# Performance work log

Measured on AMD Instinct MI355X. Metric: run time of the kernel, lower is better.

## Reference

```python
import jax, jax.numpy as jnp
import numpy as np

D = 1024; H = 16; HD = 64; L = 8; V = 2048; FF = 4096; WIN = 256
THETA = 10000.0; EPS = 1e-5; LN_EPS = 1e-5; MAXCYC = 16
NM = 16; NR = 72; NT = 12; ME = 64; RE = 64; TE = 32; TPE = 16; DE = 16
B = 2; S = 1024


def _rotate_half(x):
    # torch: stack((-x[...,1::2], x[...,0::2]), -1).flatten(-2)
    x1 = x[..., ::2]
    x2 = x[..., 1::2]
    return jnp.stack((-x2, x1), axis=-1).reshape(x.shape)


def _rmsnorm(x, w):
    return w * (x * jax.lax.rsqrt(jnp.mean(x * x, axis=-1, keepdims=True) + EPS))


def _layernorm(x, g, b):
    mu = jnp.mean(x, axis=-1, keepdims=True)
    var = jnp.mean((x - mu) ** 2, axis=-1, keepdims=True)
    return (x - mu) * jax.lax.rsqrt(var + LN_EPS) * g + b


def setup_inputs() -> dict:
    key = jax.random.key(0)
    ks = iter(jax.random.split(key, 64))
    w = lambda shape: jax.random.normal(next(ks), shape, jnp.float32) * 0.02
    inp = {
        'tokens': jax.random.randint(next(ks), (B, S), 0, V),
        'mood': jax.random.randint(next(ks), (B,), 0, NM),
        'raga': jax.random.randint(next(ks), (B,), 0, NR),
        'taal': jax.random.randint(next(ks), (B,), 0, NT),
        'tempo': jax.random.uniform(next(ks), (B,), jnp.float32),
        'duration': jax.random.uniform(next(ks), (B,), jnp.float32),
        'taal_cycle_len': 8,
        'tok_emb': w((V, D)),
        'mood_emb': w((NM, ME)), 'raga_emb': w((NR, RE)), 'taal_emb': w((NT, TE)),
        'tempo_w': w((TPE, 1)), 'tempo_b': jnp.zeros((TPE,), jnp.float32),
        'dur_w': w((DE, 1)), 'dur_b': jnp.zeros((DE,), jnp.float32),
        'proj_w': w((D, ME + RE + TE + TPE + DE)), 'proj_b': jnp.zeros((D,), jnp.float32),
        'ln_g': jnp.ones((D,), jnp.float32), 'ln_b': jnp.zeros((D,), jnp.float32),
        'cycle_emb': w((MAXCYC, D)), 'strength_emb': w((4, D)),
        'l_anorm': jnp.ones((L, D), jnp.float32), 'l_fnorm': jnp.ones((L, D), jnp.float32),
        'l_q': w((L, D, D)), 'l_k': w((L, D, D)), 'l_v': w((L, D, D)), 'l_o': w((L, D, D)),
        'l_w1': w((L, FF, D)), 'l_w2': w((L, D, FF)), 'l_w3': w((L, FF, D)),
        'final_norm': jnp.ones((D,), jnp.float32),
        'head_w': w((V, D)),
    }
    return inp


def reference(tokens, mood, raga, taal, tempo, duration, taal_cycle_len,
              tok_emb, mood_emb, raga_emb, taal_emb, tempo_w, tempo_b, dur_w, dur_b,
              proj_w, proj_b, ln_g, ln_b, cycle_emb, strength_emb,
              l_anorm, l_fnorm, l_q, l_k, l_v, l_o, l_w1, l_w2, l_w3,
              final_norm, head_w):
    bsz, seq_len = tokens.shape
    # --- ConditioningModule ---
    tp = tempo[:, None] * tempo_w[:, 0][None, :] + tempo_b      # Linear(1, TPE)
    dp = duration[:, None] * dur_w[:, 0][None, :] + dur_b       # Linear(1, DE)
    cond = jnp.concatenate([mood_emb[mood], raga_emb[raga], taal_emb[taal], tp, dp], axis=-1)
    cond = jax.nn.gelu(cond @ proj_w.T + proj_b, approximate=False)
    cond = _layernorm(cond, ln_g, ln_b)                          # [B, D]
    # --- TaalPositionEncoder (taal_cycle_len is static python int) ---
    cyc = min(int(taal_cycle_len), MAXCYC)
    pos_emb = cycle_emb[jnp.arange(seq_len) % cyc]
    strengths = jnp.full((seq_len,), 3, jnp.int32).at[::int(taal_cycle_len)].set(0)
    taal_pos = pos_emb + strength_emb[strengths]                 # [S, D]
    # --- input embedding ---
    x = tok_emb[tokens] + cond[:, None, :] + taal_pos[None]      # [B, S, D]
    # --- RoPE tables (scaling=1.0) ---
    inv_freq = 1.0 / (THETA ** (jnp.arange(0, HD, 2, jnp.float32) / HD))
    freqs = jnp.outer(jnp.arange(seq_len, dtype=jnp.float32), inv_freq)
    emb = jnp.concatenate([freqs, freqs], axis=-1)               # [S, HD]
    cos = jnp.cos(emb)[None, None]
    sin = jnp.sin(emb)[None, None]
    # --- causal sliding-window mask bias ---
    idx = jnp.arange(seq_len)
    allow = (idx[:, None] >= idx[None, :]) & (idx[:, None] - idx[None, :] < WIN)
    bias = jnp.where(allow, 0.0, -jnp.inf).astype(x.dtype)       # [S, S]
    scale = 1.0 / np.sqrt(HD)

    def block(x, p):
        an, fn, qw, kw, vw, ow, w1, w2, w3 = p
        h = _rmsnorm(x, an)
        q = (h @ qw.T).reshape(bsz, seq_len, H, HD).transpose(0, 2, 1, 3)
        k = (h @ kw.T).reshape(bsz, seq_len, H, HD).transpose(0, 2, 1, 3)
        v = (h @ vw.T).reshape(bsz, seq_len, H, HD).transpose(0, 2, 1, 3)
        q = q * cos + _rotate_half(q) * sin
        k = k * cos + _rotate_half(k) * sin
        scores = jnp.einsum('bhqd,bhkd->bhqk', q, k) * scale + bias
        attn = jax.nn.softmax(scores, axis=-1)
        y = jnp.einsum('bhqk,bhkd->bhqd', attn, v)
        y = y.transpose(0, 2, 1, 3).reshape(bsz, seq_len, D)
        x = x + y @ ow.T
        h2 = _rmsnorm(x, fn)
        x = x + (jax.nn.silu(h2 @ w1.T) * (h2 @ w3.T)) @ w2.T
        return x, None

    x, _ = jax.lax.scan(block, x, (l_anorm, l_fnorm, l_q, l_k, l_v, l_o, l_w1, l_w2, l_w3))
    x = _rmsnorm(x, final_norm)
    return x @ head_w.T                                          # [B, S, V] logits
```

## Files before the change

kernel.cpp:

```cpp
#include <hip/hip_runtime.h>
#include <math.h>

#define D_ 1024
#define H_ 16
#define HD_ 64
#define L_ 8
#define V_ 2048
#define FF_ 4096
#define WIN_ 256
#define B_ 2
#define S_ 1024
#define MAXCYC_ 16

typedef __attribute__((ext_vector_type(4))) float f32x4;
typedef __attribute__((ext_vector_type(8))) short s16x8;

__device__ __forceinline__ unsigned short f2bf(float f) {
  union { float f; unsigned int u; } v; v.f = f;
  unsigned int r = v.u + 0x7FFFu + ((v.u >> 16) & 1u);
  return (unsigned short)(r >> 16);
}

__device__ __forceinline__ float wave_sum(float v) {
  #pragma unroll
  for (int m = 1; m < 64; m <<= 1) v += __shfl_xor(v, m, 64);
  return v;
}

__device__ __forceinline__ void gload16(const unsigned short* g, unsigned short* lds) {
  __builtin_amdgcn_global_load_lds(
      (const __attribute__((address_space(1))) void*)g,
      (__attribute__((address_space(3))) void*)lds,
      16, 0, 0);
}

__global__ __launch_bounds__(256) void cvt_kernel(
    const float* __restrict__ src, unsigned short* __restrict__ dst, int n8)
{
  int i = blockIdx.x*256 + threadIdx.x;
  if (i >= n8) return;
  const float4* s = (const float4*)src + (size_t)i*2;
  float4 a = s[0], b = s[1];
  ushort4 lo, hi;
  lo.x = f2bf(a.x); lo.y = f2bf(a.y); lo.z = f2bf(a.z); lo.w = f2bf(a.w);
  hi.x = f2bf(b.x); hi.y = f2bf(b.y); hi.z = f2bf(b.z); hi.w = f2bf(b.w);
  *(ushort4*)(dst + (size_t)i*8)     = lo;
  *(ushort4*)(dst + (size_t)i*8 + 4) = hi;
}

__global__ __launch_bounds__(256) void cond_kernel(
    const int* mood, const int* raga, const int* taal,
    const float* tempo, const float* duration,
    const float* mood_emb, const float* raga_emb, const float* taal_emb,
    const float* tempo_w, const float* tempo_b, const float* dur_w, const float* dur_b,
    const float* proj_w, const float* proj_b, const float* ln_g, const float* ln_b,
    float* cond)
{
  int b = blockIdx.x;
  int t = threadIdx.x;
  __shared__ float feat[192];
  __shared__ float red[4];
  if (t < 64)        feat[t] = mood_emb[mood[b]*64 + t];
  else if (t < 128)  feat[t] = raga_emb[raga[b]*64 + (t-64)];
  else if (t < 160)  feat[t] = taal_emb[taal[b]*32 + (t-128)];
  else if (t < 176)  feat[t] = tempo[b]*tempo_w[t-160] + tempo_b[t-160];
  else if (t < 192)  feat[t] = duration[b]*dur_w[t-176] + dur_b[t-176];
  __syncthreads();
  float g[4];
  #pragma unroll
  for (int r = 0; r < 4; ++r) {
    int j = t + 256*r;
    const float* w = proj_w + (size_t)j*192;
    float acc = proj_b[j];
    for (int f = 0; f < 192; ++f) acc += feat[f]*w[f];
    g[r] = 0.5f * acc * (1.0f + erff(acc * 0.7071067811865475f));
  }
  int lane = t & 63, wv = t >> 6;
  float s1 = g[0]+g[1]+g[2]+g[3];
  s1 = wave_sum(s1);
  if (lane == 0) red[wv] = s1;
  __syncthreads();
  float mu = (red[0]+red[1]+red[2]+red[3]) * (1.0f/1024.0f);
  __syncthreads();
  float vs = 0.f;
  #pragma unroll
  for (int r = 0; r < 4; ++r) { float d = g[r]-mu; vs += d*d; }
  vs = wave_sum(vs);
  if (lane == 0) red[wv] = vs;
  __syncthreads();
  float var = (red[0]+red[1]+red[2]+red[3]) * (1.0f/1024.0f);
  float is = rsqrtf(var + 1e-5f);
  #pragma unroll
  for (int r = 0; r < 4; ++r) {
    int j = t + 256*r;
    cond[(size_t)b*D_ + j] = (g[r]-mu)*is*ln_g[j] + ln_b[j];
  }
}

__global__ __launch_bounds__(256) void embed_kernel(
    const int* tokens, const float* tok_emb, const float* cond,
    const float* cycle_emb, const float* strength_emb, const int* tcl_p, float* x)
{
  int row = blockIdx.x;
  int b = row >> 10, s = row & 1023;
  int tcl = tcl_p[0];
  int cyc = tcl < MAXCYC_ ? tcl : MAXCYC_;
  int pr  = s % cyc;
  int str = (s % tcl == 0) ? 0 : 3;
  int tok = tokens[row];
  int d = threadIdx.x * 4;
  float4 a = *(const float4*)&tok_emb[(size_t)tok*D_ + d];
  float4 c = *(const float4*)&cond[(size_t)b*D_ + d];
  float4 p = *(const float4*)&cycle_emb[(size_t)pr*D_ + d];
  float4 e = *(const float4*)&strength_emb[(size_t)str*D_ + d];
  float4 o; o.x=a.x+c.x+p.x+e.x; o.y=a.y+c.y+p.y+e.y; o.z=a.z+c.z+p.z+e.z; o.w=a.w+c.w+p.w+e.w;
  *(float4*)&x[(size_t)row*D_ + d] = o;
}

__global__ __launch_bounds__(256) void rmsnorm_kernel(
    const float* x, const float* w, unsigned short* out)
{
  int row = blockIdx.x;
  int t = threadIdx.x;
  __shared__ float red[4];
  const float* xr = x + (size_t)row*D_;
  float4 v = *(const float4*)&xr[t*4];
  float ss = v.x*v.x + v.y*v.y + v.z*v.z + v.w*v.w;
  ss = wave_sum(ss);
  int lane = t & 63, wv = t >> 6;
  if (lane == 0) red[wv] = ss;
  __syncthreads();
  float total = red[0]+red[1]+red[2]+red[3];
  float scale = rsqrtf(total * (1.0f/1024.0f) + 1e-5f);
  float4 wv4 = *(const float4*)&w[t*4];
  ushort4 o;
  o.x = f2bf(wv4.x * v.x * scale);
  o.y = f2bf(wv4.y * v.y * scale);
  o.z = f2bf(wv4.z * v.z * scale);
  o.w = f2bf(wv4.w * v.w * scale);
  *(ushort4*)&out[(size_t)row*D_ + t*4] = o;
}

__global__ __launch_bounds__(256) void resid_rmsnorm_kernel(
    float* __restrict__ x, const float* __restrict__ part, int nparts,
    const float* __restrict__ w, unsigned short* __restrict__ out)
{
  int row = blockIdx.x;
  int t = threadIdx.x;
  __shared__ float red[4];
  size_t base = (size_t)row*D_ + t*4;
  const size_t pstride = (size_t)B_*S_*D_;
  float4 v = *(const float4*)&x[base];
  for (int p = 0; p < nparts; ++p) {
    float4 a = *(const float4*)&part[p*pstride + base];
    v.x += a.x; v.y += a.y; v.z += a.z; v.w += a.w;
  }
  *(float4*)&x[base] = v;
  float ss = v.x*v.x + v.y*v.y + v.z*v.z + v.w*v.w;
  ss = wave_sum(ss);
  int lane = t & 63, wv = t >> 6;
  if (lane == 0) red[wv] = ss;
  __syncthreads();
  float total = red[0]+red[1]+red[2]+red[3];
  float scale = rsqrtf(total * (1.0f/1024.0f) + 1e-5f);
  float4 wv4 = *(const float4*)&w[t*4];
  ushort4 o;
  o.x = f2bf(wv4.x * v.x * scale);
  o.y = f2bf(wv4.y * v.y * scale);
  o.z = f2bf(wv4.z * v.z * scale);
  o.w = f2bf(wv4.w * v.w * scale);
  *(ushort4*)&out[(size_t)row*D_ + t*4] = o;
}

__global__ __launch_bounds__(256) void rope_table_kernel(float* costab, float* sintab)
{
  int i = blockIdx.x*256 + threadIdx.x;
  int s = i >> 6, d = i & 63;
  float inv = powf(10000.0f, -(float)(d & 31) * (1.0f/32.0f));
  float ang = (float)s * inv;
  float sn, cs;
  sincosf(ang, &sn, &cs);
  costab[i] = cs; sintab[i] = sn;
}

__global__ __launch_bounds__(256) void attn_mfma(
    const unsigned short* __restrict__ q, const unsigned short* __restrict__ k,
    const unsigned short* __restrict__ v, unsigned short* __restrict__ y)
{
  __shared__ unsigned short Ks[64*64];
  __shared__ unsigned short VsT[64*72];
  __shared__ unsigned short Ps[4*16*72];

  int qb0 = blockIdx.x * 64;
  int h = blockIdx.y, b = blockIdx.z;
  int t = threadIdx.x, lane = t & 63, wv = t >> 6;
  int c = lane & 15, q4 = lane >> 4;
  unsigned short* Pw = &Ps[wv*16*72];

  s16x8 aq[2];
  {
    const unsigned short* qp =
        q + ((size_t)(b*S_ + qb0 + wv*16 + c)*D_ + h*HD_ + q4*8);
    aq[0] = *(const s16x8*)qp;
    aq[1] = *(const s16x8*)(qp + 32);
  }

  f32x4 o[4];
  #pragma unroll
  for (int j = 0; j < 4; ++j) o[j] = (f32x4){0.f,0.f,0.f,0.f};
  float m[4] = {-1e30f,-1e30f,-1e30f,-1e30f};
  float l[4] = {0.f,0.f,0.f,0.f};

  int skey = t >> 2;
  int scol = (t & 3) * 16;
  int kt0 = qb0 - 256; if (kt0 < 0) kt0 = 0;

  for (int kt = kt0; kt <= qb0; kt += 64) {
    __syncthreads();
    {
      const unsigned short* kp = k + ((size_t)(b*S_ + kt + skey)*D_ + h*HD_ + scol);
      s16x8 k0 = *(const s16x8*)kp;
      s16x8 k1 = *(const s16x8*)(kp + 8);
      int ch0 = scol >> 3;
      *(s16x8*)((char*)Ks + skey*128 + ((ch0 ^ (skey & 7)) << 4)) = k0;
      *(s16x8*)((char*)Ks + skey*128 + (((ch0+1) ^ (skey & 7)) << 4)) = k1;
      const unsigned short* vp = v + ((size_t)(b*S_ + kt + skey)*D_ + h*HD_ + scol);
      s16x8 v0 = *(const s16x8*)vp;
      s16x8 v1 = *(const s16x8*)(vp + 8);
      #pragma unroll
      for (int i = 0; i < 8; ++i) {
        VsT[(scol + i)*72 + skey]     = (unsigned short)v0[i];
        VsT[(scol + 8 + i)*72 + skey] = (unsigned short)v1[i];
      }
    }
    __syncthreads();

    f32x4 sa[4];
    #pragma unroll
    for (int j = 0; j < 4; ++j) sa[j] = (f32x4){0.f,0.f,0.f,0.f};
    __builtin_amdgcn_s_setprio(1);
    #pragma unroll
    for (int ks = 0; ks < 2; ++ks)
      #pragma unroll
      for (int j = 0; j < 4; ++j) {
        int key = j*16 + c;
        s16x8 bk = *(const s16x8*)((const char*)Ks + key*128 +
                                   (((q4 + ks*4) ^ (key & 7)) << 4));
        sa[j] = __builtin_amdgcn_mfma_f32_16x16x32_bf16(aq[ks], bk, sa[j], 0, 0, 0);
      }
    __builtin_amdgcn_s_setprio(0);

    float sv[4][4];
    #pragma unroll
    for (int j = 0; j < 4; ++j) {
      int kg = kt + j*16 + c;
      #pragma unroll
      for (int reg = 0; reg < 4; ++reg) {
        int qg = qb0 + wv*16 + q4*4 + reg;
        bool ok = (qg >= kg) && (qg - kg < WIN_);
        sv[j][reg] = ok ? sa[j][reg]*0.125f : -3e38f;
      }
    }
    #pragma unroll
    for (int reg = 0; reg < 4; ++reg) {
      float mx = fmaxf(fmaxf(sv[0][reg], sv[1][reg]), fmaxf(sv[2][reg], sv[3][reg]));
      #pragma unroll
      for (int msk = 1; msk < 16; msk <<= 1)
        mx = fmaxf(mx, __shfl_xor(mx, msk, 64));
      float nm = fmaxf(m[reg], mx);
      float f = __expf(m[reg] - nm);
      m[reg] = nm;
      l[reg] *= f;
      o[0][reg] *= f; o[1][reg] *= f; o[2][reg] *= f; o[3][reg] *= f;
      float ps = 0.f;
      #pragma unroll
      for (int j = 0; j < 4; ++j) {
        float p = __expf(sv[j][reg] - nm);
        ps += p;
        Pw[(q4*4 + reg)*72 + j*16 + c] = f2bf(p);
      }
      l[reg] += ps;
    }

    __builtin_amdgcn_s_setprio(1);
    #pragma unroll
    for (int ks = 0; ks < 2; ++ks) {
      s16x8 pa = *(const s16x8*)((const char*)Pw + c*144 + (q4 + ks*4)*16);
      #pragma unroll
      for (int j = 0; j < 4; ++j) {
        s16x8 bv = *(const s16x8*)((const char*)VsT + (j*16 + c)*144 + (q4 + ks*4)*16);
        o[j] = __builtin_amdgcn_mfma_f32_16x16x32_bf16(pa, bv, o[j], 0, 0, 0);
      }
    }
    __builtin_amdgcn_s_setprio(0);
  }

  float inv[4];
  #pragma unroll
  for (int reg = 0; reg < 4; ++reg) {
    float ll = l[reg];
    #pragma unroll
    for (int msk = 1; msk < 16; msk <<= 1) ll += __shfl_xor(ll, msk, 64);
    inv[reg] = 1.0f / ll;
  }
  #pragma unroll
  for (int j = 0; j < 4; ++j)
    #pragma unroll
    for (int reg = 0; reg < 4; ++reg)
      Pw[(q4*4 + reg)*72 + j*16 + c] = f2bf(o[j][reg] * inv[reg]);
  int lr = lane >> 2, cc = (lane & 3)*16;
  s16x8 y0 = *(const s16x8*)((const char*)Pw + lr*144 + cc*2);
  s16x8 y1 = *(const s16x8*)((const char*)Pw + lr*144 + cc*2 + 16);
  unsigned short* yp = y + ((size_t)(b*S_ + qb0 + wv*16 + lr)*D_ + h*HD_ + cc);
  *(s16x8*)yp = y0;
  *(s16x8*)(yp + 8) = y1;
}

__global__ __launch_bounds__(256, 2) void gemm_w13(
    const unsigned short* __restrict__ A,
    const unsigned short* __restrict__ W1, const unsigned short* __restrict__ W3,
    unsigned short* __restrict__ T, int K, int lda, int ldw)
{
  __shared__ unsigned short sA[3][128*32];
  __shared__ unsigned short sW1[3][128*32];
  __shared__ unsigned short sW3[3][128*32];
  int tid = threadIdx.x, lane = tid & 63, wave = tid >> 6;
  int wr = (wave >> 1)*64, wc = (wave & 1)*64;
  size_t bm = (size_t)blockIdx.x*128, bn = (size_t)blockIdx.y*128;
  int fr = lane & 15, q4 = lane >> 4, fq = q4*4;
  int lrow = lane >> 2;
  int gcol = ((lane & 3) ^ ((lrow >> 1) & 3)) * 8;

  f32x4 a1[4][4], a3[4][4];
  #pragma unroll
  for (int i = 0; i < 4; ++i)
    #pragma unroll
    for (int j = 0; j < 4; ++j) {
      a1[i][j] = (f32x4){0.f,0.f,0.f,0.f};
      a3[i][j] = (f32x4){0.f,0.f,0.f,0.f};
    }

  auto stage = [&](int buf, int kt) {
    #pragma unroll
    for (int p = 0; p < 2; ++p) {
      int seg = wave*2 + p;
      size_t row = (size_t)(seg*16 + lrow);
      gload16(A  + (bm + row)*(size_t)lda + kt + gcol, &sA[buf][seg*512]);
      gload16(W1 + (bn + row)*(size_t)ldw + kt + gcol, &sW1[buf][seg*512]);
      gload16(W3 + (bn + row)*(size_t)ldw + kt + gcol, &sW3[buf][seg*512]);
    }
  };

  int nt = K >> 5;
  stage(0, 0);
  stage(1, 32);
  for (int t = 0; t < nt; ++t) {
    int cur = t % 3;
    if (t + 2 < nt) {
      stage((t+2)%3, (t+2)*32);
      asm volatile("s_waitcnt vmcnt(12)" ::: "memory");
    } else if (t + 1 < nt) {
      asm volatile("s_waitcnt vmcnt(6)" ::: "memory");
    } else {
      asm volatile("s_waitcnt vmcnt(0)" ::: "memory");
    }
    __builtin_amdgcn_sched_barrier(0);
    __builtin_amdgcn_s_barrier();
    __builtin_amdgcn_sched_barrier(0);
    s16x8 af[4], b1[4], b3[4];
    #pragma unroll
    for (int i = 0; i < 4; ++i) {
      int ra = wr + i*16 + fr, rb = wc + i*16 + fr;
      af[i] = *(const s16x8*)((const char*)&sA[cur][0]  + ra*64 + ((q4 ^ ((ra>>1)&3)) << 4));
      b1[i] = *(const s16x8*)((const char*)&sW1[cur][0] + rb*64 + ((q4 ^ ((rb>>1)&3)) << 4));
      b3[i] = *(const s16x8*)((const char*)&sW3[cur][0] + rb*64 + ((q4 ^ ((rb>>1)&3)) << 4));
    }
    __builtin_amdgcn_s_setprio(1);
    #pragma unroll
    for (int i = 0; i < 4; ++i)
      #pragma unroll
      for (int j = 0; j < 4; ++j) {
        a1[i][j] = __builtin_amdgcn_mfma_f32_16x16x32_bf16(af[i], b1[j], a1[i][j], 0, 0, 0);
        a3[i][j] = __builtin_amdgcn_mfma_f32_16x16x32_bf16(af[i], b3[j], a3[i][j], 0, 0, 0);
      }
    __builtin_amdgcn_s_setprio(0);
    __builtin_amdgcn_sched_barrier(0);
    __builtin_amdgcn_s_barrier();
    __builtin_amdgcn_sched_barrier(0);
  }

  #pragma unroll
  for (int i = 0; i < 4; ++i)
    #pragma unroll
    for (int j = 0; j < 4; ++j) {
      size_t row0 = bm + wr + i*16 + fq;
      size_t col  = bn + wc + j*16 + fr;
      #pragma unroll
      for (int qi = 0; qi < 4; ++qi) {
        float u = a1[i][j][qi];
        float g = a3[i][j][qi];
        float su = u / (1.0f + __expf(-u));
        T[(row0 + qi)*(size_t)FF_ + col] = f2bf(su * g);
      }
    }
}

template<int EPI>
__device__ __forceinline__ void gemm64_core(
    const unsigned short* __restrict__ A, const unsigned short* __restrict__ W,
    float* __restrict__ Cf, unsigned short* __restrict__ Cb,
    int kbase, int Kslice, int lda, int ldw, int ldc,
    const float* __restrict__ costab, const float* __restrict__ sintab)
{
  __shared__ unsigned short sA[3][128*32];
  __shared__ unsigned short sW[3][64*32];
  int tid = threadIdx.x, lane = tid & 63, wave = tid >> 6;
  int wr = (wave >> 1)*64, wc = (wave & 1)*32;
  size_t bm = (size_t)blockIdx.x*128, bn = (size_t)blockIdx.y*64;
  int fr = lane & 15, q4 = lane >> 4, fq = q4*4;
  int lrow = lane >> 2;
  int gcol = ((lane & 3) ^ ((lrow >> 1) & 3)) * 8;

  f32x4 acc[4][2];
  #pragma unroll
  for (int i = 0; i < 4; ++i) {
    acc[i][0] = (f32x4){0.f,0.f,0.f,0.f};
    acc[i][1] = (f32x4){0.f,0.f,0.f,0.f};
  }

  auto stage = [&](int buf, int kt) {
    #pragma unroll
    for (int p = 0; p < 2; ++p) {
      int seg = wave*2 + p;
      gload16(A + (bm + seg*16 + lrow)*(size_t)lda + kt + gcol, &sA[buf][seg*512]);
    }
    gload16(W + (bn + wave*16 + lrow)*(size_t)ldw + kt + gcol, &sW[buf][wave*512]);
  };

  int nt = Kslice >> 5;
  stage(0, kbase);
  stage(1, kbase + 32);
  for (int t = 0; t < nt; ++t) {
    int cur = t % 3;
    if (t + 2 < nt) {
      stage((t+2)%3, kbase + (t+2)*32);
      asm volatile("s_waitcnt vmcnt(6)" ::: "memory");
    } else if (t + 1 < nt) {
      asm volatile("s_waitcnt vmcnt(3)" ::: "memory");
    } else {
      asm volatile("s_waitcnt vmcnt(0)" ::: "memory");
    }
    __builtin_amdgcn_sched_barrier(0);
    __builtin_amdgcn_s_barrier();
    __builtin_amdgcn_sched_barrier(0);
    s16x8 af[4], bw[2];
    #pragma unroll
    for (int i = 0; i < 4; ++i) {
      int r = wr + i*16 + fr;
      af[i] = *(const s16x8*)((const char*)&sA[cur][0] + r*64 + ((q4 ^ ((r>>1)&3)) << 4));
    }
    #pragma unroll
    for (int j = 0; j < 2; ++j) {
      int r = wc + j*16 + fr;
      bw[j] = *(const s16x8*)((const char*)&sW[cur][0] + r*64 + ((q4 ^ ((r>>1)&3)) << 4));
    }
    __builtin_amdgcn_s_setprio(1);
    #pragma unroll
    for (int i = 0; i < 4; ++i)
      #pragma unroll
      for (int j = 0; j < 2; ++j)
        acc[i][j] = __builtin_amdgcn_mfma_f32_16x16x32_bf16(af[i], bw[j], acc[i][j], 0, 0, 0);
    __builtin_amdgcn_s_setprio(0);
    __builtin_amdgcn_sched_barrier(0);
    __builtin_amdgcn_s_barrier();
    __builtin_amdgcn_sched_barrier(0);
  }

  #pragma unroll
  for (int i = 0; i < 4; ++i)
    #pragma unroll
    for (int j = 0; j < 2; ++j) {
      size_t row0 = bm + wr + i*16 + fq;
      size_t col  = bn + wc + j*16 + fr;
      #pragma unroll
      for (int qi = 0; qi < 4; ++qi) {
        float val = acc[i][j][qi];
        size_t idx = (row0 + qi)*(size_t)ldc + col;
        if (EPI == 3) {
          float pv = __shfl_xor(val, 1, 64);
          int srow = (int)((row0 + qi) & 1023);
          int d = (int)(col & 63);
          float cs = costab[srow*64 + d];
          float sn = sintab[srow*64 + d];
          Cb[idx] = f2bf(val*cs + ((d & 1) ? pv : -pv)*sn);
        } else if (EPI == 4) {
          Cb[idx] = f2bf(val);
        } else {
          Cf[idx] = val;
        }
      }
    }
}

template<int EPI>
__global__ __launch_bounds__(256, 3) void gemm64(
    const unsigned short* __restrict__ A, const unsigned short* __restrict__ W,
    float* __restrict__ Cf, int K, int lda, int ldw, int ldc)
{
  gemm64_core<EPI>(A, W, Cf, nullptr, 0, K, lda, ldw, ldc, nullptr, nullptr);
}

__global__ __launch_bounds__(256, 3) void gemm64_ksplit(
    const unsigned short* __restrict__ A, const unsigned short* __restrict__ W,
    float* __restrict__ P, int Kslice, int lda, int ldw, int ldc)
{
  float* out = P + (size_t)blockIdx.z * (size_t)B_ * S_ * ldc;
  gemm64_core<0>(A, W, out, nullptr, blockIdx.z*Kslice, Kslice, lda, ldw, ldc,
                 nullptr, nullptr);
}

__global__ __launch_bounds__(256, 3) void gemm_qkv64(
    const unsigned short* __restrict__ A,
    const unsigned short* __restrict__ Wq, const unsigned short* __restrict__ Wk,
    const unsigned short* __restrict__ Wv,
    unsigned short* __restrict__ Cq, unsigned short* __restrict__ Ck,
    unsigned short* __restrict__ Cv,
    const float* __restrict__ costab, const float* __restrict__ sintab)
{
  if (blockIdx.z == 0)
    gemm64_core<3>(A, Wq, nullptr, Cq, 0, D_, D_, D_, D_, costab, sintab);
  else if (blockIdx.z == 1)
    gemm64_core<3>(A, Wk, nullptr, Ck, 0, D_, D_, D_, D_, costab, sintab);
  else
    gemm64_core<4>(A, Wv, nullptr, Cv, 0, D_, D_, D_, D_, nullptr, nullptr);
}

extern "C" void kernel_launch(void* const* d_in, const int* in_sizes, int n_in,
                              void* d_out, int out_size, void* d_ws, size_t ws_size,
                              hipStream_t stream)
{
  const int*   tokens    = (const int*)d_in[0];
  const int*   mood      = (const int*)d_in[1];
  const int*   raga      = (const int*)d_in[2];
  const int*   taal      = (const int*)d_in[3];
  const float* tempo     = (const float*)d_in[4];
  const float* duration  = (const float*)d_in[5];
  const int*   tcl       = (const int*)d_in[6];
  const float* tok_emb   = (const float*)d_in[7];
  const float* mood_emb  = (const float*)d_in[8];
  const float* raga_emb  = (const float*)d_in[9];
  const float* taal_emb  = (const float*)d_in[10];
  const float* tempo_w   = (const float*)d_in[11];
  const float* tempo_b   = (const float*)d_in[12];
  const float* dur_w     = (const float*)d_in[13];
  const float* dur_b     = (const float*)d_in[14];
  const float* proj_w    = (const float*)d_in[15];
  const float* proj_b    = (const float*)d_in[16];
  const float* ln_g      = (const float*)d_in[17];
  const float* ln_b      = (const float*)d_in[18];
  const float* cycle_emb = (const float*)d_in[19];
  const float* strength_e= (const float*)d_in[20];
  const float* l_anorm   = (const float*)d_in[21];
  const float* l_fnorm   = (const float*)d_in[22];
  const float* l_q       = (const float*)d_in[23];
  const float* l_k       = (const float*)d_in[24];
  const float* l_v       = (const float*)d_in[25];
  const float* l_o       = (const float*)d_in[26];
  const float* l_w1      = (const float*)d_in[27];
  const float* l_w2      = (const float*)d_in[28];
  const float* l_w3      = (const float*)d_in[29];
  const float* final_norm= (const float*)d_in[30];
  const float* head_w    = (const float*)d_in[31];

  size_t off = 0;
  char* wsb = (char*)d_ws;
  auto alloc = [&](size_t bytes) -> char* {
    char* p = wsb + off;
    off += (bytes + 255) & ~(size_t)255;
    return p;
  };
  float*          condb  = (float*)alloc((size_t)B_*D_*4);
  float*          costab = (float*)alloc((size_t)S_*HD_*4);
  float*          sintab = (float*)alloc((size_t)S_*HD_*4);
  float*          x      = (float*)alloc((size_t)B_*S_*D_*4);
  unsigned short* hbuf   = (unsigned short*)alloc((size_t)B_*S_*D_*2);
  unsigned short* qb     = (unsigned short*)alloc((size_t)B_*S_*D_*2);
  unsigned short* kb     = (unsigned short*)alloc((size_t)B_*S_*D_*2);
  unsigned short* vb     = (unsigned short*)alloc((size_t)B_*S_*D_*2);
  unsigned short* yb     = (unsigned short*)alloc((size_t)B_*S_*D_*2);
  unsigned short* tb     = (unsigned short*)alloc((size_t)B_*S_*FF_*2);
  float*          pbuf   = (float*)alloc((size_t)4*B_*S_*D_*4);

  const size_t N_QKVO = (size_t)L_*D_*D_;
  const size_t N_FF   = (size_t)L_*FF_*D_;
  const size_t N_HEAD = (size_t)V_*D_;
  unsigned short* wbf = (unsigned short*)alloc((4*N_QKVO + 3*N_FF + N_HEAD)*2);
  unsigned short* bq = wbf;
  unsigned short* bk = wbf + N_QKVO;
  unsigned short* bv = wbf + 2*N_QKVO;
  unsigned short* bo = wbf + 3*N_QKVO;
  unsigned short* b1 = wbf + 4*N_QKVO;
  unsigned short* b2 = wbf + 4*N_QKVO + N_FF;
  unsigned short* b3 = wbf + 4*N_QKVO + 2*N_FF;
  unsigned short* bh = wbf + 4*N_QKVO + 3*N_FF;

  rope_table_kernel<<<(S_*HD_)/256, 256, 0, stream>>>(costab, sintab);
  cond_kernel<<<B_, 256, 0, stream>>>(mood, raga, taal, tempo, duration,
      mood_emb, raga_emb, taal_emb, tempo_w, tempo_b, dur_w, dur_b,
      proj_w, proj_b, ln_g, ln_b, condb);
  embed_kernel<<<B_*S_, 256, 0, stream>>>(tokens, tok_emb, condb, cycle_emb,
      strength_e, tcl, x);

  cvt_kernel<<<(int)(N_QKVO/8/256), 256, 0, stream>>>(l_q,  bq, (int)(N_QKVO/8));
  cvt_kernel<<<(int)(N_QKVO/8/256), 256, 0, stream>>>(l_k,  bk, (int)(N_QKVO/8));
  cvt_kernel<<<(int)(N_QKVO/8/256), 256, 0, stream>>>(l_v,  bv, (int)(N_QKVO/8));
  cvt_kernel<<<(int)(N_QKVO/8/256), 256, 0, stream>>>(l_o,  bo, (int)(N_QKVO/8));
  cvt_kernel<<<(int)(N_FF/8/256),   256, 0, stream>>>(l_w1, b1, (int)(N_FF/8));
  cvt_kernel<<<(int)(N_FF/8/256),   256, 0, stream>>>(l_w2, b2, (int)(N_FF/8));
  cvt_kernel<<<(int)(N_FF/8/256),   256, 0, stream>>>(l_w3, b3, (int)(N_FF/8));
  cvt_kernel<<<(int)(N_HEAD/8/256), 256, 0, stream>>>(head_w, bh, (int)(N_HEAD/8));

  const int rows = B_*S_;
  rmsnorm_kernel<<<rows, 256, 0, stream>>>(x, l_anorm, hbuf);
  for (int l = 0; l < L_; ++l) {
    size_t dd = (size_t)l*D_*D_;
    size_t fd = (size_t)l*FF_*D_;
    gemm_qkv64<<<dim3(rows/128, D_/64, 3), 256, 0, stream>>>(
        hbuf, bq + dd, bk + dd, bv + dd, qb, kb, vb, costab, sintab);
    attn_mfma<<<dim3(S_/64, H_, B_), 256, 0, stream>>>(qb, kb, vb, yb);
    gemm64_ksplit<<<dim3(rows/128, D_/64, 2), 256, 0, stream>>>(
        yb, bo + dd, pbuf, 512, D_, D_, D_);
    resid_rmsnorm_kernel<<<rows, 256, 0, stream>>>(
        x, pbuf, 2, l_fnorm + (size_t)l*D_, hbuf);
    gemm_w13<<<dim3(rows/128, FF_/128), 256, 0, stream>>>(
        hbuf, b1 + fd, b3 + fd, tb, D_, D_, D_);
    gemm64_ksplit<<<dim3(rows/128, D_/64, 4), 256, 0, stream>>>(
        tb, b2 + fd, pbuf, 1024, FF_, FF_, D_);
    const float* nextw = (l+1 < L_) ? (l_anorm + (size_t)(l+1)*D_) : final_norm;
    resid_rmsnorm_kernel<<<rows, 256, 0, stream>>>(x, pbuf, 4, nextw, hbuf);
  }
  gemm64<0><<<dim3(rows/128, V_/64), 256, 0, stream>>>(
      hbuf, bh, (float*)d_out, D_, D_, D_, V_);
}
```

Measured before the change: 1.583 ms.

## Widen GEMM tiles to 128x128 and process 128 queries per attention block

The shared GEMM core moves from 128x64 to 128x128 output tiles, giving each wave a 4x4 grid of MFMA accumulators and more operand reuse per LDS load. The wait counts and grid sizes are updated to match. The output-projection k-split grows from 2 to 4 slices so the grid stays large enough, and the residual kernel now sums 4 partials. Attention blocks now cover 128 queries with two 16-row groups per wave, so K/V tiles are shared by twice as many queries, and waves skip tiles outside their window. The costs are higher register pressure, fewer blocks per launch (the attention grid is halved), and extra partial-sum traffic for the output projection.

New measurement: 1.717 ms. 8.4% more time.

```diff
diff --git a/kernel.cpp b/kernel.cpp
--- a/kernel.cpp
+++ b/kernel.cpp
@@ -189,33 +189,41 @@
 {
   __shared__ unsigned short Ks[64*64];
   __shared__ unsigned short VsT[64*72];
-  __shared__ unsigned short Ps[4*16*72];
-
-  int qb0 = blockIdx.x * 64;
+  __shared__ unsigned short Ps[4*32*72];
+
+  int qb0 = blockIdx.x * 128;
   int h = blockIdx.y, b = blockIdx.z;
   int t = threadIdx.x, lane = t & 63, wv = t >> 6;
   int c = lane & 15, q4 = lane >> 4;
-  unsigned short* Pw = &Ps[wv*16*72];
-
-  s16x8 aq[2];
-  {
+  unsigned short* Pw = &Ps[wv*32*72];
+  int qbase = qb0 + wv*32;
+
+  s16x8 aq[2][2];
+  #pragma unroll
+  for (int rg = 0; rg < 2; ++rg) {
     const unsigned short* qp =
-        q + ((size_t)(b*S_ + qb0 + wv*16 + c)*D_ + h*HD_ + q4*8);
-    aq[0] = *(const s16x8*)qp;
-    aq[1] = *(const s16x8*)(qp + 32);
-  }
-
-  f32x4 o[4];
-  #pragma unroll
-  for (int j = 0; j < 4; ++j) o[j] = (f32x4){0.f,0.f,0.f,0.f};
-  float m[4] = {-1e30f,-1e30f,-1e30f,-1e30f};
-  float l[4] = {0.f,0.f,0.f,0.f};
+        q + ((size_t)(b*S_ + qbase + rg*16 + c)*D_ + h*HD_ + q4*8);
+    aq[rg][0] = *(const s16x8*)qp;
+    aq[rg][1] = *(const s16x8*)(qp + 32);
+  }
+
+  f32x4 o[2][4];
+  float m[2][4], l[2][4];
+  #pragma unroll
+  for (int rg = 0; rg < 2; ++rg)
+    #pragma unroll
+    for (int j = 0; j < 4; ++j) {
+      o[rg][j] = (f32x4){0.f,0.f,0.f,0.f};
+      m[rg][j] = -1e30f; l[rg][j] = 0.f;
+    }
 
   int skey = t >> 2;
   int scol = (t & 3) * 16;
-  int kt0 = qb0 - 256; if (kt0 < 0) kt0 = 0;
-
-  for (int kt = kt0; kt <= qb0; kt += 64) {
+  int kt0 = qb0 - (WIN_-1); if (kt0 < 0) kt0 = 0;
+  kt0 &= ~63;
+  int ktend = qb0 + 64;
+
+  for (int kt = kt0; kt <= ktend; kt += 64) {
     __syncthreads();
     {
       const unsigned short* kp = k + ((size_t)(b*S_ + kt + skey)*D_ + h*HD_ + scol);
@@ -235,85 +243,94 @@
     }
     __syncthreads();
 
-    f32x4 sa[4];
-    #pragma unroll
-    for (int j = 0; j < 4; ++j) sa[j] = (f32x4){0.f,0.f,0.f,0.f};
-    __builtin_amdgcn_s_setprio(1);
-    #pragma unroll
-    for (int ks = 0; ks < 2; ++ks)
+    if (kt > qbase + 31 || kt + 63 < qbase - (WIN_-1)) continue;
+
+    #pragma unroll
+    for (int rg = 0; rg < 2; ++rg) {
+      f32x4 sa[4];
+      #pragma unroll
+      for (int j = 0; j < 4; ++j) sa[j] = (f32x4){0.f,0.f,0.f,0.f};
+      __builtin_amdgcn_s_setprio(1);
+      #pragma unroll
+      for (int ks = 0; ks < 2; ++ks)
+        #pragma unroll
+        for (int j = 0; j < 4; ++j) {
+          int key = j*16 + c;
+          s16x8 bk = *(const s16x8*)((const char*)Ks + key*128 +
+                                     (((q4 + ks*4) ^ (key & 7)) << 4));
+          sa[j] = __builtin_amdgcn_mfma_f32_16x16x32_bf16(aq[rg][ks], bk, sa[j], 0, 0, 0);
+        }
+      __builtin_amdgcn_s_setprio(0);
+
+      float sv[4][4];
       #pragma unroll
       for (int j = 0; j < 4; ++j) {
-        int key = j*16 + c;
-        s16x8 bk = *(const s16x8*)((const char*)Ks + key*128 +
-                                   (((q4 + ks*4) ^ (key & 7)) << 4));
-        sa[j] = __builtin_amdgcn_mfma_f32_16x16x32_bf16(aq[ks], bk, sa[j], 0, 0, 0);
+        int kg = kt + j*16 + c;
+        #pragma unroll
+        for (int reg = 0; reg < 4; ++reg) {
+          int qg = qbase + rg*16 + q4*4 + reg;
+          bool ok = (qg >= kg) && (qg - kg < WIN_);
+          sv[j][reg] = ok ? sa[j][reg]*0.125f : -3e38f;
+        }
       }
-    __builtin_amdgcn_s_setprio(0);
-
-    float sv[4][4];
-    #pragma unroll
-    for (int j = 0; j < 4; ++j) {
-      int kg = kt + j*16 + c;
       #pragma unroll
       for (int reg = 0; reg < 4; ++reg) {
-        int qg = qb0 + wv*16 + q4*4 + reg;
-        bool ok = (qg >= kg) && (qg - kg < WIN_);
-        sv[j][reg] = ok ? sa[j][reg]*0.125f : -3e38f;
+        float mx = fmaxf(fmaxf(sv[0][reg], sv[1][reg]), fmaxf(sv[2][reg], sv[3][reg]));
+        #pragma unroll
+        for (int msk = 1; msk < 16; msk <<= 1)
+          mx = fmaxf(mx, __shfl_xor(mx, msk, 64));
+        float nm = fmaxf(m[rg][reg], mx);
+        float f = __expf(m[rg][reg] - nm);
+        m[rg][reg] = nm;
+        l[rg][reg] *= f;
+        o[rg][0][reg] *= f; o[rg][1][reg] *= f;
+        o[rg][2][reg] *= f; o[rg][3][reg] *= f;
+        float ps = 0.f;
+        #pragma unroll
+        for (int j = 0; j < 4; ++j) {
+          float p = __expf(sv[j][reg] - nm);
+          ps += p;
+          Pw[(rg*16 + q4*4 + reg)*72 + j*16 + c] = f2bf(p);
+        }
+        l[rg][reg] += ps;
       }
-    }
+
+      __builtin_amdgcn_s_setprio(1);
+      #pragma unroll
+      for (int ks = 0; ks < 2; ++ks) {
+        s16x8 pa = *(const s16x8*)((const char*)Pw + (rg*16 + c)*144 + (q4 + ks*4)*16);
+        #pragma unroll
+        for (int j = 0; j < 4; ++j) {
+          s16x8 bv = *(const s16x8*)((const char*)VsT + (j*16 + c)*144 + (q4 + ks*4)*16);
+          o[rg][j] = __builtin_amdgcn_mfma_f32_16x16x32_bf16(pa, bv, o[rg][j], 0, 0, 0);
+        }
+      }
+      __builtin_amdgcn_s_setprio(0);
+    }
+  }
+
+  #pragma unroll
+  for (int rg = 0; rg < 2; ++rg) {
     #pragma unroll
     for (int reg = 0; reg < 4; ++reg) {
-      float mx = fmaxf(fmaxf(sv[0][reg], sv[1][reg]), fmaxf(sv[2][reg], sv[3][reg]));
-      #pragma unroll
-      for (int msk = 1; msk < 16; msk <<= 1)
-        mx = fmaxf(mx, __shfl_xor(mx, msk, 64));
-      float nm = fmaxf(m[reg], mx);
-      float f = __expf(m[reg] - nm);
-      m[reg] = nm;
-      l[reg] *= f;
-      o[0][reg] *= f; o[1][reg] *= f; o[2][reg] *= f; o[3][reg] *= f;
-      float ps = 0.f;
-      #pragma unroll
-      for (int j = 0; j < 4; ++j) {
-        float p = __expf(sv[j][reg] - nm);
-        ps += p;
-        Pw[(q4*4 + reg)*72 + j*16 + c] = f2bf(p);
-      }
-      l[reg] += ps;
-    }
-
-    __builtin_amdgcn_s_setprio(1);
-    #pragma unroll
-    for (int ks = 0; ks < 2; ++ks) {
-      s16x8 pa = *(const s16x8*)((const char*)Pw + c*144 + (q4 + ks*4)*16);
-      #pragma unroll
-      for (int j = 0; j < 4; ++j) {
-        s16x8 bv = *(const s16x8*)((const char*)VsT + (j*16 + c)*144 + (q4 + ks*4)*16);
-        o[j] = __builtin_amdgcn_mfma_f32_16x16x32_bf16(pa, bv, o[j], 0, 0, 0);
-      }
-    }
-    __builtin_amdgcn_s_setprio(0);
-  }
-
-  float inv[4];
-  #pragma unroll
-  for (int reg = 0; reg < 4; ++reg) {
-    float ll = l[reg];
-    #pragma unroll
-    for (int msk = 1; msk < 16; msk <<= 1) ll += __shfl_xor(ll, msk, 64);
-    inv[reg] = 1.0f / ll;
-  }
-  #pragma unroll
-  for (int j = 0; j < 4; ++j)
-    #pragma unroll
-    for (int reg = 0; reg < 4; ++reg)
-      Pw[(q4*4 + reg)*72 + j*16 + c] = f2bf(o[j][reg] * inv[reg]);
+      float ll = l[rg][reg];
+      #pragma unroll
+      for (int msk = 1; msk < 16; msk <<= 1) ll += __shfl_xor(ll, msk, 64);
+      float inv = 1.0f / ll;
+      #pragma unroll
+      for (int j = 0; j < 4; ++j)
+        Pw[(rg*16 + q4*4 + reg)*72 + j*16 + c] = f2bf(o[rg][j][reg] * inv);
+    }
+  }
   int lr = lane >> 2, cc = (lane & 3)*16;
-  s16x8 y0 = *(const s16x8*)((const char*)Pw + lr*144 + cc*2);
-  s16x8 y1 = *(const s16x8*)((const char*)Pw + lr*144 + cc*2 + 16);
-  unsigned short* yp = y + ((size_t)(b*S_ + qb0 + wv*16 + lr)*D_ + h*HD_ + cc);
-  *(s16x8*)yp = y0;
-  *(s16x8*)(yp + 8) = y1;
+  #pragma unroll
+  for (int rg = 0; rg < 2; ++rg) {
+    s16x8 y0 = *(const s16x8*)((const char*)Pw + (rg*16 + lr)*144 + cc*2);
+    s16x8 y1 = *(const s16x8*)((const char*)Pw + (rg*16 + lr)*144 + cc*2 + 16);
+    unsigned short* yp = y + ((size_t)(b*S_ + qbase + rg*16 + lr)*D_ + h*HD_ + cc);
+    *(s16x8*)yp = y0;
+    *(s16x8*)(yp + 8) = y1;
+  }
 }
 
 __global__ __launch_bounds__(256, 2) void gemm_w13(
@@ -406,35 +423,36 @@
 }
 
 template<int EPI>
-__device__ __forceinline__ void gemm64_core(
+__device__ __forceinline__ void gemm128_core(
     const unsigned short* __restrict__ A, const unsigned short* __restrict__ W,
     float* __restrict__ Cf, unsigned short* __restrict__ Cb,
     int kbase, int Kslice, int lda, int ldw, int ldc,
     const float* __restrict__ costab, const float* __restrict__ sintab)
 {
   __shared__ unsigned short sA[3][128*32];
-  __shared__ unsigned short sW[3][64*32];
+  __shared__ unsigned short sW[3][128*32];
   int tid = threadIdx.x, lane = tid & 63, wave = tid >> 6;
-  int wr = (wave >> 1)*64, wc = (wave & 1)*32;
-  size_t bm = (size_t)blockIdx.x*128, bn = (size_t)blockIdx.y*64;
+  int wr = (wave >> 1)*64, wc = (wave & 1)*64;
+  size_t bm = (size_t)blockIdx.x*128, bn = (size_t)blockIdx.y*128;
   int fr = lane & 15, q4 = lane >> 4, fq = q4*4;
   int lrow = lane >> 2;
   int gcol = ((lane & 3) ^ ((lrow >> 1) & 3)) * 8;
 
-  f32x4 acc[4][2];
-  #pragma unroll
-  for (int i = 0; i < 4; ++i) {
-    acc[i][0] = (f32x4){0.f,0.f,0.f,0.f};
-    acc[i][1] = (f32x4){0.f,0.f,0.f,0.f};
-  }
+  f32x4 acc[4][4];
+  #pragma unroll
+  for (int i = 0; i < 4; ++i)
+    #pragma unroll
+    for (int j = 0; j < 4; ++j)
+      acc[i][j] = (f32x4){0.f,0.f,0.f,0.f};
 
   auto stage = [&](int buf, int kt) {
     #pragma unroll
     for (int p = 0; p < 2; ++p) {
       int seg = wave*2 + p;
-      gload16(A + (bm + seg*16 + lrow)*(size_t)lda + kt + gcol, &sA[buf][seg*512]);
-    }
-    gload16(W + (bn + wave*16 + lrow)*(size_t)ldw + kt + gcol, &sW[buf][wave*512]);
+      size_t row = (size_t)(seg*16 + lrow);
+      gload16(A + (bm + row)*(size_t)lda + kt + gcol, &sA[buf][seg*512]);
+      gload16(W + (bn + row)*(size_t)ldw + kt + gcol, &sW[buf][seg*512]);
+    }
   };
 
   int nt = Kslice >> 5;
@@ -444,31 +462,27 @@
     int cur = t % 3;
     if (t + 2 < nt) {
       stage((t+2)%3, kbase + (t+2)*32);
-      asm volatile("s_waitcnt vmcnt(6)" ::: "memory");
+      asm volatile("s_waitcnt vmcnt(8)" ::: "memory");
     } else if (t + 1 < nt) {
-      asm volatile("s_waitcnt vmcnt(3)" ::: "memory");
+      asm volatile("s_waitcnt vmcnt(4)" ::: "memory");
     } else {
       asm volatile("s_waitcnt vmcnt(0)" ::: "memory");
     }
     __builtin_amdgcn_sched_barrier(0);
     __builtin_amdgcn_s_barrier();
     __builtin_amdgcn_sched_barrier(0);
-    s16x8 af[4], bw[2];
+    s16x8 af[4], bw[4];
     #pragma unroll
     for (int i = 0; i < 4; ++i) {
-      int r = wr + i*16 + fr;
-      af[i] = *(const s16x8*)((const char*)&sA[cur][0] + r*64 + ((q4 ^ ((r>>1)&3)) << 4));
-    }
-    #pragma unroll
-    for (int j = 0; j < 2; ++j) {
-      int r = wc + j*16 + fr;
-      bw[j] = *(const s16x8*)((const char*)&sW[cur][0] + r*64 + ((q4 ^ ((r>>1)&3)) << 4));
+      int ra = wr + i*16 + fr, rb = wc + i*16 + fr;
+      af[i] = *(const s16x8*)((const char*)&sA[cur][0] + ra*64 + ((q4 ^ ((ra>>1)&3)) << 4));
+      bw[i] = *(const s16x8*)((const char*)&sW[cur][0] + rb*64 + ((q4 ^ ((rb>>1)&3)) << 4));
     }
     __builtin_amdgcn_s_setprio(1);
     #pragma unroll
     for (int i = 0; i < 4; ++i)
       #pragma unroll
-      for (int j = 0; j < 2; ++j)
+      for (int j = 0; j < 4; ++j)
         acc[i][j] = __builtin_amdgcn_mfma_f32_16x16x32_bf16(af[i], bw[j], acc[i][j], 0, 0, 0);
     __builtin_amdgcn_s_setprio(0);
     __builtin_amdgcn_sched_barrier(0);
@@ -479,7 +493,7 @@
   #pragma unroll
   for (int i = 0; i < 4; ++i)
     #pragma unroll
-    for (int j = 0; j < 2; ++j) {
+    for (int j = 0; j < 4; ++j) {
       size_t row0 = bm + wr + i*16 + fq;
       size_t col  = bn + wc + j*16 + fr;
       #pragma unroll
@@ -503,23 +517,23 @@
 }
 
 template<int EPI>
-__global__ __launch_bounds__(256, 3) void gemm64(
+__global__ __launch_bounds__(256, 3) void gemm128(
     const unsigned short* __restrict__ A, const unsigned short* __restrict__ W,
     float* __restrict__ Cf, int K, int lda, int ldw, int ldc)
 {
-  gemm64_core<EPI>(A, W, Cf, nullptr, 0, K, lda, ldw, ldc, nullptr, nullptr);
-}
-
-__global__ __launch_bounds__(256, 3) void gemm64_ksplit(
+  gemm128_core<EPI>(A, W, Cf, nullptr, 0, K, lda, ldw, ldc, nullptr, nullptr);
+}
+
+__global__ __launch_bounds__(256, 3) void gemm128_ksplit(
     const unsigned short* __restrict__ A, const unsigned short* __restrict__ W,
     float* __restrict__ P, int Kslice, int lda, int ldw, int ldc)
 {
   float* out = P + (size_t)blockIdx.z * (size_t)B_ * S_ * ldc;
-  gemm64_core<0>(A, W, out, nullptr, blockIdx.z*Kslice, Kslice, lda, ldw, ldc,
-                 nullptr, nullptr);
-}
-
-__global__ __launch_bounds__(256, 3) void gemm_qkv64(
+  gemm128_core<0>(A, W, out, nullptr, blockIdx.z*Kslice, Kslice, lda, ldw, ldc,
+                  nullptr, nullptr);
+}
+
+__global__ __launch_bounds__(256, 3) void gemm_qkv128(
     const unsigned short* __restrict__ A,
     const unsigned short* __restrict__ Wq, const unsigned short* __restrict__ Wk,
     const unsigned short* __restrict__ Wv,
@@ -528,11 +542,11 @@
     const float* __restrict__ costab, const float* __restrict__ sintab)
 {
   if (blockIdx.z == 0)
-    gemm64_core<3>(A, Wq, nullptr, Cq, 0, D_, D_, D_, D_, costab, sintab);
+    gemm128_core<3>(A, Wq, nullptr, Cq, 0, D_, D_, D_, D_, costab, sintab);
   else if (blockIdx.z == 1)
-    gemm64_core<3>(A, Wk, nullptr, Ck, 0, D_, D_, D_, D_, costab, sintab);
+    gemm128_core<3>(A, Wk, nullptr, Ck, 0, D_, D_, D_, D_, costab, sintab);
   else
-    gemm64_core<4>(A, Wv, nullptr, Cv, 0, D_, D_, D_, D_, nullptr, nullptr);
+    gemm128_core<4>(A, Wv, nullptr, Cv, 0, D_, D_, D_, D_, nullptr, nullptr);
 }
 
 extern "C" void kernel_launch(void* const* d_in, const int* in_sizes, int n_in,
@@ -625,20 +639,20 @@
   for (int l = 0; l < L_; ++l) {
     size_t dd = (size_t)l*D_*D_;
     size_t fd = (size_t)l*FF_*D_;
-    gemm_qkv64<<<dim3(rows/128, D_/64, 3), 256, 0, stream>>>(
+    gemm_qkv128<<<dim3(rows/128, D_/128, 3), 256, 0, stream>>>(
         hbuf, bq + dd, bk + dd, bv + dd, qb, kb, vb, costab, sintab);
-    attn_mfma<<<dim3(S_/64, H_, B_), 256, 0, stream>>>(qb, kb, vb, yb);
-    gemm64_ksplit<<<dim3(rows/128, D_/64, 2), 256, 0, stream>>>(
-        yb, bo + dd, pbuf, 512, D_, D_, D_);
+    attn_mfma<<<dim3(S_/128, H_, B_), 256, 0, stream>>>(qb, kb, vb, yb);
+    gemm128_ksplit<<<dim3(rows/128, D_/128, 4), 256, 0, stream>>>(
+        yb, bo + dd, pbuf, 256, D_, D_, D_);
     resid_rmsnorm_kernel<<<rows, 256, 0, stream>>>(
-        x, pbuf, 2, l_fnorm + (size_t)l*D_, hbuf);
+        x, pbuf, 4, l_fnorm + (size_t)l*D_, hbuf);
     gemm_w13<<<dim3(rows/128, FF_/128), 256, 0, stream>>>(
         hbuf, b1 + fd, b3 + fd, tb, D_, D_, D_);
-    gemm64_ksplit<<<dim3(rows/128, D_/64, 4), 256, 0, stream>>>(
+    gemm128_ksplit<<<dim3(rows/128, D_/128, 4), 256, 0, stream>>>(
         tb, b2 + fd, pbuf, 1024, FF_, FF_, D_);
     const float* nextw = (l+1 < L_) ? (l_anorm + (size_t)(l+1)*D_) : final_norm;
     resid_rmsnorm_kernel<<<rows, 256, 0, stream>>>(x, pbuf, 4, nextw, hbuf);
   }
-  gemm64<0><<<dim3(rows/128, V_/64), 256, 0, stream>>>(
+  gemm128<0><<<dim3(rows/128, V_/128), 256, 0, stream>>>(
       hbuf, bh, (float*)d_out, D_, D_, D_, V_);
 }
```
